# Kernel tuning notes

Hardware: AMD Instinct MI355X
Metric: run time of the kernel (lower is better)

The kernel has to match this reference:

```python
import jax, jax.numpy as jnp
import numpy as np
import math

D_MODEL = 512
N_HEADS = 8
K_NEIGHBORS = 30
B, S = 4, 2048
N_VARIATES = 8
EPS = 1e-5


def layer_norm(x, g, b):
    m = jnp.mean(x, axis=-1, keepdims=True)
    v = jnp.mean(jnp.square(x - m), axis=-1, keepdims=True)
    return (x - m) * jax.lax.rsqrt(v + EPS) * g + b


def mha(x, mask, w_in, b_in, w_out, b_out):
    # x: [B,S,D]; mask: [B,S,S] bool, True = blocked (same for every head)
    Bb, Ss, D = x.shape
    H, dh = N_HEADS, D // N_HEADS
    qkv = x @ w_in.T + b_in                      # [B,S,3D]
    q, k, v = jnp.split(qkv, 3, axis=-1)
    q = q.reshape(Bb, Ss, H, dh).transpose(0, 2, 1, 3)
    k = k.reshape(Bb, Ss, H, dh).transpose(0, 2, 1, 3)
    v = v.reshape(Bb, Ss, H, dh).transpose(0, 2, 1, 3)
    scores = jnp.einsum('bhqd,bhkd->bhqk', q, k) / math.sqrt(dh)
    scores = jnp.where(mask[:, None, :, :], -jnp.inf, scores)
    attn = jax.nn.softmax(scores, axis=-1)
    o = jnp.einsum('bhqk,bhkd->bhqd', attn, v)
    o = o.transpose(0, 2, 1, 3).reshape(Bb, Ss, D)
    return o @ w_out.T + b_out


def build_masks(variates, times, valid_mask):
    Bb, Ss = variates.shape
    eye = jnp.eye(Ss, dtype=bool)
    same_var = variates[:, :, None] == variates[:, None, :]      # [B,S,S]
    valid_2d = valid_mask[:, :, None] & valid_mask[:, None, :]
    intra_mask = ~(same_var & valid_2d)                          # True = blocked
    blocked_i = jnp.any(jnp.all(intra_mask, axis=-1))
    intra_mask = intra_mask & ~(blocked_i & eye)                 # unblock diagonal if any row fully blocked

    diff_var = ~same_var
    time_dist = jnp.abs(times[:, :, None] - times[:, None, :])
    time_dist = jnp.where(~valid_2d | ~diff_var, jnp.inf, time_dist)
    k = min(K_NEIGHBORS, Ss)
    _, topk_idx = jax.lax.top_k(-time_dist, k)                   # k smallest distances
    b_idx = jnp.arange(Bb)[:, None, None]
    r_idx = jnp.arange(Ss)[None, :, None]
    knn_mask = jnp.zeros((Bb, Ss, Ss), dtype=bool).at[b_idx, r_idx, topk_idx].set(True)
    knn_mask = knn_mask & valid_2d
    inter_mask = ~knn_mask
    blocked_e = jnp.any(jnp.all(inter_mask, axis=-1))
    inter_mask = inter_mask & ~(blocked_e & eye)
    return intra_mask, inter_mask


def setup_inputs() -> dict:
    key = jax.random.key(0)
    ks = jax.random.split(key, 12)
    D = D_MODEL
    s = 0.02
    inp = {
        'x': jax.random.normal(ks[0], (B, S, D), dtype=jnp.float32),
        'variates': jax.random.randint(ks[1], (B, S), 0, N_VARIATES),
        'times': jax.random.uniform(ks[2], (B, S), dtype=jnp.float32),
        'valid_mask': jnp.ones((B, S), dtype=bool),
        'in_w1': jax.random.normal(ks[3], (3 * D, D), dtype=jnp.float32) * s,
        'in_b1': jnp.zeros((3 * D,), dtype=jnp.float32),
        'out_w1': jax.random.normal(ks[4], (D, D), dtype=jnp.float32) * s,
        'out_b1': jnp.zeros((D,), dtype=jnp.float32),
        'ln_g1': jnp.ones((D,), dtype=jnp.float32),
        'ln_b1': jnp.zeros((D,), dtype=jnp.float32),
        'in_w2': jax.random.normal(ks[5], (3 * D, D), dtype=jnp.float32) * s,
        'in_b2': jnp.zeros((3 * D,), dtype=jnp.float32),
        'out_w2': jax.random.normal(ks[6], (D, D), dtype=jnp.float32) * s,
        'out_b2': jnp.zeros((D,), dtype=jnp.float32),
        'ln_g2': jnp.ones((D,), dtype=jnp.float32),
        'ln_b2': jnp.zeros((D,), dtype=jnp.float32),
    }
    return inp


def reference(x, variates, times, valid_mask,
              in_w1, in_b1, out_w1, out_b1, ln_g1, ln_b1,
              in_w2, in_b2, out_w2, out_b2, ln_g2, ln_b2):
    intra_mask, inter_mask = build_masks(variates, times, valid_mask)
    a1 = mha(x, intra_mask, in_w1, in_b1, out_w1, out_b1)
    x = layer_norm(x + a1, ln_g1, ln_b1)
    a2 = mha(x, inter_mask, in_w2, in_b2, out_w2, out_b2)
    x = layer_norm(x + a2, ln_g2, ln_b2)
    return x
```

## Files before the change

### kernel.cpp

```cpp
#include <hip/hip_runtime.h>


#define S_LEN 2048
#define BATCH 4
#define DM    512
#define NH    8
#define DH    64
#define KNN_K 30
#define NVAR  8
#define NTOK  (BATCH * S_LEN)
#define QKVD  (3 * DM)
#define PADCAP 2560
#define MAXTILE 40

typedef float f32x4 __attribute__((ext_vector_type(4)));
typedef short s16x8 __attribute__((ext_vector_type(8)));
typedef short s16x4 __attribute__((ext_vector_type(4)));

__device__ __forceinline__ float bf2f(short u) {
  return __uint_as_float(((unsigned)(unsigned short)u) << 16);
}
__device__ __forceinline__ short f2bf(float f) {
  unsigned x = __float_as_uint(f);
  return (short)((x + 0x7fffu + ((x >> 16) & 1u)) >> 16);
}

#define KNNB (NTOK / 8)
#define C_N0 (NTOK * DM / 4)
#define C_N1 (QKVD * DM / 4)
#define C_N2 (DM * DM / 4)
#define C_B1 (C_N0 + C_N1)
#define C_B2 (C_B1 + C_N2)
#define C_B3 (C_B2 + C_N1)
#define C_B4 (C_B3 + C_N2)
#define PREP_GRID (KNNB + BATCH + C_B4 / 256)

__global__ __launch_bounds__(256) void prep_all(
    const int* __restrict__ variates, const float* __restrict__ times,
    int* __restrict__ knn_out,
    int* __restrict__ gcnt, int* __restrict__ pgoff, int* __restrict__ porig,
    int* __restrict__ tileV, int* __restrict__ tileQ0, int* __restrict__ ntile,
    const float* __restrict__ s0, const float* __restrict__ s1,
    const float* __restrict__ s2, const float* __restrict__ s3,
    const float* __restrict__ s4, short* __restrict__ d0,
    short* __restrict__ d1, short* __restrict__ d2,
    short* __restrict__ d3, short* __restrict__ d4) {
  int blk = blockIdx.x;
  int tid = threadIdx.x;

  if (blk < KNNB) {
    int w = tid >> 6, lane = tid & 63;
    int bq0 = blk * 8 + w * 2;
    int bq1 = bq0 + 1;
    int b = bq0 >> 11;
    float tq0 = times[bq0], tq1 = times[bq1];
    int vq0 = variates[bq0], vq1 = variates[bq1];
    const float* tb = times + b * S_LEN;
    const int* vb = variates + b * S_LEN;
    int j0 = lane * 32;

    unsigned u0[32], u1[32];
#pragma unroll
    for (int q = 0; q < 8; ++q) {
      float4 t4 = *(const float4*)(tb + j0 + q * 4);
      int4 v4 = *(const int4*)(vb + j0 + q * 4);
      u0[q * 4 + 0] = __float_as_uint((v4.x == vq0) ? __builtin_inff() : fabsf(tq0 - t4.x));
      u0[q * 4 + 1] = __float_as_uint((v4.y == vq0) ? __builtin_inff() : fabsf(tq0 - t4.y));
      u0[q * 4 + 2] = __float_as_uint((v4.z == vq0) ? __builtin_inff() : fabsf(tq0 - t4.z));
      u0[q * 4 + 3] = __float_as_uint((v4.w == vq0) ? __builtin_inff() : fabsf(tq0 - t4.w));
      u1[q * 4 + 0] = __float_as_uint((v4.x == vq1) ? __builtin_inff() : fabsf(tq1 - t4.x));
      u1[q * 4 + 1] = __float_as_uint((v4.y == vq1) ? __builtin_inff() : fabsf(tq1 - t4.y));
      u1[q * 4 + 2] = __float_as_uint((v4.z == vq1) ? __builtin_inff() : fabsf(tq1 - t4.z));
      u1[q * 4 + 3] = __float_as_uint((v4.w == vq1) ? __builtin_inff() : fabsf(tq1 - t4.w));
    }

    unsigned lo0 = 0u, hi0 = 0x7F800000u;
    unsigned lo1 = 0u, hi1 = 0x7F800000u;
    for (int it = 0; it < 31; ++it) {
      unsigned mid0 = lo0 + ((hi0 - lo0) >> 1);
      unsigned mid1 = lo1 + ((hi1 - lo1) >> 1);
      int c0 = 0, c1 = 0;
#pragma unroll
      for (int k = 0; k < 32; ++k) {
        c0 += (u0[k] <= mid0) ? 1 : 0;
        c1 += (u1[k] <= mid1) ? 1 : 0;
      }
      int pc = c0 | (c1 << 16);
#pragma unroll
      for (int o2 = 32; o2; o2 >>= 1) pc += __shfl_xor(pc, o2);
      int pc0 = pc & 0xffff, pc1 = pc >> 16;
      if (lo0 < hi0) { if (pc0 >= KNN_K) hi0 = mid0; else lo0 = mid0 + 1; }
      if (lo1 < hi1) { if (pc1 >= KNN_K) hi1 = mid1; else lo1 = mid1 + 1; }
    }
    unsigned tau0 = lo0, tau1 = lo1;

    int cl0 = 0, ce0 = 0, cl1 = 0, ce1 = 0;
#pragma unroll
    for (int k = 0; k < 32; ++k) {
      cl0 += (u0[k] < tau0) ? 1 : 0;  ce0 += (u0[k] == tau0) ? 1 : 0;
      cl1 += (u1[k] < tau1) ? 1 : 0;  ce1 += (u1[k] == tau1) ? 1 : 0;
    }
    int pa = cl0 | (cl1 << 16), pe = ce0 | (ce1 << 16);
#pragma unroll
    for (int o2 = 1; o2 < 64; o2 <<= 1) {
      int ta = __shfl_up(pa, o2);
      int te = __shfl_up(pe, o2);
      if (lane >= o2) { pa += ta; pe += te; }
    }
    int paTop = __shfl(pa, 63);
    int totL0 = paTop & 0xffff, totL1 = paTop >> 16;
    int excl0 = (pa & 0xffff) - cl0, excl1 = (pa >> 16) - cl1;
    int exce0 = totL0 + (pe & 0xffff) - ce0, exce1 = totL1 + (pe >> 16) - ce1;

    int* op0 = knn_out + bq0 * KNN_K;
    int* op1 = knn_out + bq1 * KNN_K;
    int pos0 = excl0, pos1 = excl1;
#pragma unroll
    for (int k = 0; k < 32; ++k) {
      if (u0[k] < tau0) { op0[pos0] = j0 + k; ++pos0; }
      if (u1[k] < tau1) { op1[pos1] = j0 + k; ++pos1; }
    }
    int r0 = exce0, r1 = exce1;
#pragma unroll
    for (int k = 0; k < 32; ++k) {
      if (u0[k] == tau0) { if (r0 < KNN_K) op0[r0] = j0 + k; ++r0; }
      if (u1[k] == tau1) { if (r1 < KNN_K) op1[r1] = j0 + k; ++r1; }
    }
  } else if (blk < KNNB + BATCH) {
    int b = blk - KNNB;
    int t = tid;
    __shared__ int scnt[64][NVAR];
    __shared__ int soff[64][NVAR];
    __shared__ int stot[NVAR], sbase[NVAR];
    for (int p = t; p < PADCAP; p += 256) porig[b * PADCAP + p] = -1;
    const int* vb = variates + b * S_LEN;
    int c[NVAR] = {0, 0, 0, 0, 0, 0, 0, 0};
    if (t < 64) {
      for (int j = t * 32; j < t * 32 + 32; ++j) {
        int v = vb[j];
#pragma unroll
        for (int u = 0; u < NVAR; ++u) c[u] += (v == u);
      }
#pragma unroll
      for (int u = 0; u < NVAR; ++u) scnt[t][u] = c[u];
    }
    __syncthreads();
    if (t < NVAR) {
      int a = 0;
      for (int u = 0; u < 64; ++u) { soff[u][t] = a; a += scnt[u][t]; }
      stot[t] = a;
    }
    __syncthreads();
    if (t == 0) {
      int a = 0, nt = 0;
      for (int v = 0; v < NVAR; ++v) {
        sbase[v] = a;
        pgoff[b * NVAR + v] = a;
        gcnt[b * NVAR + v] = stot[v];
        int ntv = (stot[v] + 63) >> 6;
        for (int i = 0; i < ntv; ++i) {
          tileV[b * MAXTILE + nt] = v;
          tileQ0[b * MAXTILE + nt] = a + i * 64;
          ++nt;
        }
        a += ntv * 64;
      }
      ntile[b] = nt;
    }
    __syncthreads();
    if (t < 64) {
      int o[NVAR];
#pragma unroll
      for (int u = 0; u < NVAR; ++u) o[u] = sbase[u] + soff[t][u];
      for (int j = t * 32; j < t * 32 + 32; ++j) {
        int v = vb[j];
        int dst = 0;
#pragma unroll
        for (int u = 0; u < NVAR; ++u) dst += (v == u) ? o[u] : 0;
        porig[b * PADCAP + dst] = j;
#pragma unroll
        for (int u = 0; u < NVAR; ++u) o[u] += (v == u);
      }
    }
  } else {
    int i = (blk - KNNB - BATCH) * 256 + tid;
    const float* src; short* dst; int k;
    if (i < C_N0)      { src = s0; dst = d0; k = i; }
    else if (i < C_B1) { src = s1; dst = d1; k = i - C_N0; }
    else if (i < C_B2) { src = s2; dst = d2; k = i - C_B1; }
    else if (i < C_B3) { src = s3; dst = d3; k = i - C_B2; }
    else               { src = s4; dst = d4; k = i - C_B3; }
    float4 v = ((const float4*)src)[k];
    s16x4 o;
    o[0] = f2bf(v.x); o[1] = f2bf(v.y); o[2] = f2bf(v.z); o[3] = f2bf(v.w);
    ((s16x4*)dst)[k] = o;
  }
}

template <int OUT_BF16>
__global__ __launch_bounds__(256) void gemm_bt(const short* __restrict__ A,
                                               const short* __restrict__ Bm,
                                               const float* __restrict__ bias,
                                               void* __restrict__ Cout,
                                               int M, int N, int K) {
  __shared__ short sA[128 * 40];
  __shared__ short sB[128 * 40];
  int n0 = blockIdx.x * 128, m0 = blockIdx.y * 128;
  int tid = threadIdx.x;
  int lane = tid & 63, wv = tid >> 6;
  int wr = wv >> 1, wc = wv & 1;

  int srow = tid >> 2;
  int scol = (tid & 3) * 8;
  const short* aG = A + (size_t)(m0 + srow) * K + scol;
  const short* bG = Bm + (size_t)(n0 + srow) * K + scol;

  f32x4 acc[4][4] = {};
  int nk = K >> 5;

  s16x8 pa0 = *(const s16x8*)(aG);
  s16x8 pa1 = *(const s16x8*)(aG + (size_t)64 * K);
  s16x8 pb0 = *(const s16x8*)(bG);
  s16x8 pb1 = *(const s16x8*)(bG + (size_t)64 * K);

  for (int kt = 0; kt < nk; ++kt) {
    __syncthreads();
    *(s16x8*)&sA[srow * 40 + scol] = pa0;
    *(s16x8*)&sA[(srow + 64) * 40 + scol] = pa1;
    *(s16x8*)&sB[srow * 40 + scol] = pb0;
    *(s16x8*)&sB[(srow + 64) * 40 + scol] = pb1;
    __syncthreads();
    if (kt + 1 < nk) {
      const short* a2 = aG + (kt + 1) * 32;
      const short* b2 = bG + (kt + 1) * 32;
      pa0 = *(const s16x8*)(a2);
      pa1 = *(const s16x8*)(a2 + (size_t)64 * K);
      pb0 = *(const s16x8*)(b2);
      pb1 = *(const s16x8*)(b2 + (size_t)64 * K);
    }
    int kb = (lane >> 4) * 8;
    int ar = wr * 64 + (lane & 15);
    int br = wc * 64 + (lane & 15);
    s16x8 af[4], bf[4];
#pragma unroll
    for (int m = 0; m < 4; ++m) af[m] = *(const s16x8*)&sA[(ar + m * 16) * 40 + kb];
#pragma unroll
    for (int n = 0; n < 4; ++n) bf[n] = *(const s16x8*)&sB[(br + n * 16) * 40 + kb];
#pragma unroll
    for (int m = 0; m < 4; ++m)
#pragma unroll
      for (int n = 0; n < 4; ++n)
        acc[m][n] = __builtin_amdgcn_mfma_f32_16x16x32_bf16(af[m], bf[n], acc[m][n], 0, 0, 0);
  }

  int crow0 = m0 + wr * 64 + ((lane >> 4) * 4);
  int ccol0 = n0 + wc * 64 + (lane & 15);
#pragma unroll
  for (int n = 0; n < 4; ++n) {
    int col = ccol0 + n * 16;
    float bv = bias ? bias[col] : 0.f;
#pragma unroll
    for (int m = 0; m < 4; ++m) {
#pragma unroll
      for (int j = 0; j < 4; ++j) {
        int row = crow0 + m * 16 + j;
        float val = acc[m][n][j] + bv;
        if (OUT_BF16)
          ((short*)Cout)[(size_t)row * N + col] = f2bf(val);
        else
          ((float*)Cout)[(size_t)row * N + col] = val;
      }
    }
  }
}

__global__ __launch_bounds__(192) void permute_qkv(const short* __restrict__ qkvb,
                                                   const int* __restrict__ porig,
                                                   short* __restrict__ pq) {
  int row = blockIdx.x;
  int b = row / PADCAP;
  int orig = porig[row];
  int t = threadIdx.x;
  s16x8 val;
  if (orig >= 0) {
    val = *(const s16x8*)(qkvb + ((size_t)(b * S_LEN + orig)) * QKVD + t * 8);
    if (t < 64) {
#pragma unroll
      for (int i = 0; i < 8; ++i) val[i] = f2bf(bf2f(val[i]) * 0.125f);
    }
  } else {
#pragma unroll
    for (int i = 0; i < 8; ++i) val[i] = 0;
  }
  *(s16x8*)(pq + (size_t)row * QKVD + t * 8) = val;
}

__global__ __launch_bounds__(256) void intra_attn(
    const short* __restrict__ pq, const int* __restrict__ porig,
    const int* __restrict__ tileV, const int* __restrict__ tileQ0,
    const int* __restrict__ ntile, const int* __restrict__ pgoff,
    const int* __restrict__ gcnt, short* __restrict__ o) {
  int b = blockIdx.z, h = blockIdx.y, t = blockIdx.x;
  if (t >= ntile[b]) return;
  int v = tileV[b * MAXTILE + t];
  int q0 = tileQ0[b * MAXTILE + t];
  int k0 = pgoff[b * NVAR + v];
  int L = gcnt[b * NVAR + v];
  int nch = (L + 63) >> 6;

  __shared__ short sQ[2][64][40];
  __shared__ short sK[2][64][40];
  __shared__ short sVT[2][64][40];
  __shared__ short sP[2][64][40];

  int tid = threadIdx.x, lane = tid & 63, w = tid >> 6;
  int colbase = lane & 15;
  int kfrag = (lane >> 4) * 8;

  {
    int r = tid >> 2, cc = (tid & 3) * 16;
    const short* src = pq + ((size_t)(b * PADCAP + q0 + r)) * QKVD + h * DH + cc;
    s16x8 v0 = *(const s16x8*)src;
    s16x8 v1 = *(const s16x8*)(src + 8);
    int half = cc >> 5, kk = cc & 31;
    *(s16x8*)&sQ[half][r][kk] = v0;
    *(s16x8*)&sQ[half][r][kk + 8] = v1;
  }

  f32x4 accO[4] = {};
  float mrun[4], lrun[4];
#pragma unroll
  for (int j = 0; j < 4; ++j) { mrun[j] = -__builtin_inff(); lrun[j] = 0.f; }

  for (int c = 0; c < nch; ++c) {
    __syncthreads();
    {
      int r = tid >> 2, cc = (tid & 3) * 16;
      size_t rowg = (size_t)(b * PADCAP + k0 + c * 64 + r) * QKVD;
      const short* srcK = pq + rowg + DM + h * DH + cc;
      s16x8 k0v = *(const s16x8*)srcK;
      s16x8 k1v = *(const s16x8*)(srcK + 8);
      int half = cc >> 5, kk = cc & 31;
      *(s16x8*)&sK[half][r][kk] = k0v;
      *(s16x8*)&sK[half][r][kk + 8] = k1v;
      const short* srcV = pq + rowg + 2 * DM + h * DH + cc;
      s16x8 v0v = *(const s16x8*)srcV;
      s16x8 v1v = *(const s16x8*)(srcV + 8);
      int khalf = r >> 5, kkv = r & 31;
#pragma unroll
      for (int i = 0; i < 8; ++i) sVT[khalf][cc + i][kkv] = v0v[i];
#pragma unroll
      for (int i = 0; i < 8; ++i) sVT[khalf][cc + 8 + i][kkv] = v1v[i];
    }
    __syncthreads();

    s16x8 aQ0 = *(const s16x8*)&sQ[0][w * 16 + colbase][kfrag];
    s16x8 aQ1 = *(const s16x8*)&sQ[1][w * 16 + colbase][kfrag];
    f32x4 accS[4] = {};
#pragma unroll
    for (int n = 0; n < 4; ++n) {
      s16x8 b0 = *(const s16x8*)&sK[0][n * 16 + colbase][kfrag];
      s16x8 b1 = *(const s16x8*)&sK[1][n * 16 + colbase][kfrag];
      accS[n] = __builtin_amdgcn_mfma_f32_16x16x32_bf16(aQ0, b0, accS[n], 0, 0, 0);
      accS[n] = __builtin_amdgcn_mfma_f32_16x16x32_bf16(aQ1, b1, accS[n], 0, 0, 0);
    }

    float pv[4][4];
#pragma unroll
    for (int j = 0; j < 4; ++j) {
      float cm = -__builtin_inff();
#pragma unroll
      for (int n = 0; n < 4; ++n) {
        bool ok = (c * 64 + n * 16 + colbase) < L;
        float se = ok ? accS[n][j] : -__builtin_inff();
        cm = fmaxf(cm, se);
      }
      for (int o2 = 8; o2; o2 >>= 1) cm = fmaxf(cm, __shfl_xor(cm, o2));
      float mn = fmaxf(mrun[j], cm);
      float al = __expf(mrun[j] - mn);
      float rs = 0.f;
#pragma unroll
      for (int n = 0; n < 4; ++n) {
        bool ok = (c * 64 + n * 16 + colbase) < L;
        float p = ok ? __expf(accS[n][j] - mn) : 0.f;
        pv[n][j] = p;
        rs += p;
      }
      for (int o2 = 8; o2; o2 >>= 1) rs += __shfl_xor(rs, o2);
      lrun[j] = lrun[j] * al + rs;
      mrun[j] = mn;
#pragma unroll
      for (int n = 0; n < 4; ++n) accO[n][j] *= al;
    }

    int prow = w * 16 + ((lane >> 4) << 2);
#pragma unroll
    for (int n = 0; n < 4; ++n)
#pragma unroll
      for (int j = 0; j < 4; ++j)
        sP[n >> 1][prow + j][colbase + ((n & 1) << 4)] = f2bf(pv[n][j]);

    s16x8 aP0 = *(const s16x8*)&sP[0][w * 16 + colbase][kfrag];
    s16x8 aP1 = *(const s16x8*)&sP[1][w * 16 + colbase][kfrag];
#pragma unroll
    for (int n = 0; n < 4; ++n) {
      s16x8 b0 = *(const s16x8*)&sVT[0][n * 16 + colbase][kfrag];
      s16x8 b1 = *(const s16x8*)&sVT[1][n * 16 + colbase][kfrag];
      accO[n] = __builtin_amdgcn_mfma_f32_16x16x32_bf16(aP0, b0, accO[n], 0, 0, 0);
      accO[n] = __builtin_amdgcn_mfma_f32_16x16x32_bf16(aP1, b1, accO[n], 0, 0, 0);
    }
  }

#pragma unroll
  for (int j = 0; j < 4; ++j) {
    int prow = w * 16 + (lane >> 4) * 4 + j;
    int orig = porig[b * PADCAP + q0 + prow];
    if (orig >= 0) {
      float inv = 1.f / lrun[j];
      size_t base = ((size_t)(b * S_LEN + orig)) * DM + h * DH;
#pragma unroll
      for (int n = 0; n < 4; ++n)
        o[base + n * 16 + colbase] = f2bf(accO[n][j] * inv);
    }
  }
}

__global__ __launch_bounds__(256) void inter_attn(const short* __restrict__ qkv,
                                                  const int* __restrict__ knn,
                                                  short* __restrict__ o) {
  __shared__ float sS[4][NH][32];
  __shared__ float sP[4][NH][32];
  int tid = threadIdx.x, lane = tid & 63, w = tid >> 6;
  int bq = blockIdx.x * 4 + w;
  int b = bq >> 11;
  int h = lane >> 3;

  int myidx = (lane < KNN_K) ? knn[bq * KNN_K + lane] : 0;

  s16x8 q8 = *(const s16x8*)(qkv + (size_t)bq * QKVD + lane * 8);
  float qf[8];
#pragma unroll
  for (int i = 0; i < 8; ++i) qf[i] = bf2f(q8[i]) * 0.125f;

  for (int j = 0; j < KNN_K; ++j) {
    int idx = __shfl(myidx, j);
    s16x8 k8 = *(const s16x8*)(qkv + ((size_t)(b * S_LEN + idx)) * QKVD + DM + lane * 8);
    float acc = 0.f;
#pragma unroll
    for (int i = 0; i < 8; ++i) acc += qf[i] * bf2f(k8[i]);
    acc += __shfl_xor(acc, 1);
    acc += __shfl_xor(acc, 2);
    acc += __shfl_xor(acc, 4);
    if ((lane & 7) == 0) sS[w][h][j] = acc;
  }

  int jsub = lane & 7;
  float sv0 = sS[w][h][jsub];
  float sv1 = sS[w][h][jsub + 8];
  float sv2 = sS[w][h][jsub + 16];
  float sv3 = (jsub < 6) ? sS[w][h][jsub + 24] : -__builtin_inff();
  float m = fmaxf(fmaxf(sv0, sv1), fmaxf(sv2, sv3));
  m = fmaxf(m, __shfl_xor(m, 1));
  m = fmaxf(m, __shfl_xor(m, 2));
  m = fmaxf(m, __shfl_xor(m, 4));
  float p0 = __expf(sv0 - m), p1 = __expf(sv1 - m), p2 = __expf(sv2 - m);
  float p3 = (jsub < 6) ? __expf(sv3 - m) : 0.f;
  sP[w][h][jsub] = p0;
  sP[w][h][jsub + 8] = p1;
  sP[w][h][jsub + 16] = p2;
  sP[w][h][jsub + 24] = p3;
  float l = p0 + p1 + p2 + p3;
  l += __shfl_xor(l, 1);
  l += __shfl_xor(l, 2);
  l += __shfl_xor(l, 4);

  float o8[8] = {};
  for (int j = 0; j < KNN_K; ++j) {
    int idx = __shfl(myidx, j);
    s16x8 v8 = *(const s16x8*)(qkv + ((size_t)(b * S_LEN + idx)) * QKVD + 2 * DM + lane * 8);
    float p = sP[w][h][j];
#pragma unroll
    for (int i = 0; i < 8; ++i) o8[i] += p * bf2f(v8[i]);
  }
  float inv = 1.f / l;
  s16x8 ov;
#pragma unroll
  for (int i = 0; i < 8; ++i) ov[i] = f2bf(o8[i] * inv);
  *(s16x8*)(o + (size_t)bq * DM + lane * 8) = ov;
}

__global__ __launch_bounds__(256) void residual_ln(const float* __restrict__ x,
                                                   const float* __restrict__ a,
                                                   const float* __restrict__ g,
                                                   const float* __restrict__ bta,
                                                   float* __restrict__ yf,
                                                   short* __restrict__ yb) {
  int row = blockIdx.x * 4 + (threadIdx.x >> 6);
  int lane = threadIdx.x & 63;
  const float4* xp = (const float4*)(x + (size_t)row * DM);
  const float4* ap = (const float4*)(a + (size_t)row * DM);
  float4 v0 = xp[lane * 2], v1 = xp[lane * 2 + 1];
  float4 a0 = ap[lane * 2], a1 = ap[lane * 2 + 1];
  float r[8] = {v0.x + a0.x, v0.y + a0.y, v0.z + a0.z, v0.w + a0.w,
                v1.x + a1.x, v1.y + a1.y, v1.z + a1.z, v1.w + a1.w};
  float s = 0.f;
#pragma unroll
  for (int j = 0; j < 8; ++j) s += r[j];
  for (int o2 = 32; o2; o2 >>= 1) s += __shfl_xor(s, o2);
  float mean = s * (1.f / DM);
  float vs = 0.f;
#pragma unroll
  for (int j = 0; j < 8; ++j) { float d = r[j] - mean; vs += d * d; }
  for (int o2 = 32; o2; o2 >>= 1) vs += __shfl_xor(vs, o2);
  float inv = rsqrtf(vs * (1.f / DM) + 1e-5f);
  const float4* gp = (const float4*)g;
  const float4* bp = (const float4*)bta;
  float4 g0 = gp[lane * 2], g1 = gp[lane * 2 + 1];
  float4 b0 = bp[lane * 2], b1 = bp[lane * 2 + 1];
  float gg[8] = {g0.x, g0.y, g0.z, g0.w, g1.x, g1.y, g1.z, g1.w};
  float bb[8] = {b0.x, b0.y, b0.z, b0.w, b1.x, b1.y, b1.z, b1.w};
  float y[8];
#pragma unroll
  for (int j = 0; j < 8; ++j) y[j] = (r[j] - mean) * inv * gg[j] + bb[j];
  float4 o0 = {y[0], y[1], y[2], y[3]};
  float4 o1 = {y[4], y[5], y[6], y[7]};
  float4* yp = (float4*)(yf + (size_t)row * DM);
  yp[lane * 2] = o0;
  yp[lane * 2 + 1] = o1;
  if (yb) {
    s16x8 ob;
#pragma unroll
    for (int j = 0; j < 8; ++j) ob[j] = f2bf(y[j]);
    *(s16x8*)(yb + (size_t)row * DM + lane * 8) = ob;
  }
}

extern "C" void kernel_launch(void* const* d_in, const int* in_sizes, int n_in,
                              void* d_out, int out_size, void* d_ws, size_t ws_size,
                              hipStream_t stream) {
  const float* x      = (const float*)d_in[0];
  const int*   var    = (const int*)d_in[1];
  const float* times  = (const float*)d_in[2];
  const float* in_w1  = (const float*)d_in[4];
  const float* in_b1  = (const float*)d_in[5];
  const float* out_w1 = (const float*)d_in[6];
  const float* out_b1 = (const float*)d_in[7];
  const float* ln_g1  = (const float*)d_in[8];
  const float* ln_b1  = (const float*)d_in[9];
  const float* in_w2  = (const float*)d_in[10];
  const float* in_b2  = (const float*)d_in[11];
  const float* out_w2 = (const float*)d_in[12];
  const float* out_b2 = (const float*)d_in[13];
  const float* ln_g2  = (const float*)d_in[14];
  const float* ln_b2  = (const float*)d_in[15];
  float* out = (float*)d_out;

  char* ws = (char*)d_ws;
  size_t off = 0;
  auto alloc = [&](size_t bytes) -> char* {
    char* p = ws + off;
    off = (off + bytes + 255) & ~(size_t)255;
    return p;
  };
  short* xb    = (short*)alloc((size_t)NTOK * DM * 2);
  short* x1b   = (short*)alloc((size_t)NTOK * DM * 2);
  short* w1q   = (short*)alloc((size_t)QKVD * DM * 2);
  short* w1o   = (short*)alloc((size_t)DM * DM * 2);
  short* w2q   = (short*)alloc((size_t)QKVD * DM * 2);
  short* w2o   = (short*)alloc((size_t)DM * DM * 2);
  short* qkvb  = (short*)alloc((size_t)NTOK * QKVD * 2);
  short* ob    = (short*)alloc((size_t)NTOK * DM * 2);
  char*  region = alloc((size_t)NTOK * DM * 4 * 2);
  float* af    = (float*)region;
  float* x1f   = (float*)(region + (size_t)NTOK * DM * 4);
  short* pqkv  = (short*)region;
  int* gcnt    = (int*)alloc((size_t)BATCH * NVAR * 4);
  int* pgoff   = (int*)alloc((size_t)BATCH * NVAR * 4);
  int* porig   = (int*)alloc((size_t)BATCH * PADCAP * 4);
  int* tileV   = (int*)alloc((size_t)BATCH * MAXTILE * 4);
  int* tileQ0  = (int*)alloc((size_t)BATCH * MAXTILE * 4);
  int* ntile   = (int*)alloc((size_t)BATCH * 4);
  int* knn     = (int*)alloc((size_t)NTOK * KNN_K * 4);

  prep_all<<<PREP_GRID, 256, 0, stream>>>(
      var, times, knn, gcnt, pgoff, porig, tileV, tileQ0, ntile,
      x, in_w1, out_w1, in_w2, out_w2, xb, w1q, w1o, w2q, w2o);

  gemm_bt<1><<<dim3(QKVD / 128, NTOK / 128), 256, 0, stream>>>(xb, w1q, in_b1, qkvb,
                                                               NTOK, QKVD, DM);
  permute_qkv<<<BATCH * PADCAP, 192, 0, stream>>>(qkvb, porig, pqkv);
  intra_attn<<<dim3(MAXTILE, NH, BATCH), 256, 0, stream>>>(pqkv, porig, tileV, tileQ0,
                                                           ntile, pgoff, gcnt, ob);
  gemm_bt<0><<<dim3(DM / 128, NTOK / 128), 256, 0, stream>>>(ob, w1o, out_b1, af,
                                                             NTOK, DM, DM);
  residual_ln<<<NTOK / 4, 256, 0, stream>>>(x, af, ln_g1, ln_b1, x1f, x1b);

  gemm_bt<1><<<dim3(QKVD / 128, NTOK / 128), 256, 0, stream>>>(x1b, w2q, in_b2, qkvb,
                                                               NTOK, QKVD, DM);
  inter_attn<<<NTOK / 4, 256, 0, stream>>>(qkvb, knn, ob);
  gemm_bt<0><<<dim3(DM / 128, NTOK / 128), 256, 0, stream>>>(ob, w2o, out_b2, af,
                                                             NTOK, DM, DM);
  residual_ln<<<NTOK / 4, 256, 0, stream>>>(x1f, af, ln_g2, ln_b2, out, nullptr);
}
```

Baseline: 226.3 us.

## Gather QKV rows in intra-attention directly and stop kNN bisection early

Removes the permute_qkv kernel, which copied QKV rows into variate-grouped padded order with Q pre-scaled. intra_attn now looks up each row's original token through porig and loads Q/K/V straight from the GEMM output, and applies the 1/sqrt(dh) scale to the scores in fp32. This saves a full launch plus a write and read of the permuted buffer, at the cost of scattered gathers inside attention. Padded rows are clamped to token 0, which the existing length mask is relied on to exclude. The kNN threshold bisection also now exits once both searches have converged.

After: 220.8 us. 1.02x faster.

```diff
diff --git a/kernel.cpp b/kernel.cpp
--- a/kernel.cpp
+++ b/kernel.cpp
@@ -91,6 +91,7 @@
       int pc0 = pc & 0xffff, pc1 = pc >> 16;
       if (lo0 < hi0) { if (pc0 >= KNN_K) hi0 = mid0; else lo0 = mid0 + 1; }
       if (lo1 < hi1) { if (pc1 >= KNN_K) hi1 = mid1; else lo1 = mid1 + 1; }
+      if (lo0 >= hi0 && lo1 >= hi1) break;
     }
     unsigned tau0 = lo0, tau1 = lo1;
 
@@ -274,29 +275,8 @@
   }
 }
 
-__global__ __launch_bounds__(192) void permute_qkv(const short* __restrict__ qkvb,
-                                                   const int* __restrict__ porig,
-                                                   short* __restrict__ pq) {
-  int row = blockIdx.x;
-  int b = row / PADCAP;
-  int orig = porig[row];
-  int t = threadIdx.x;
-  s16x8 val;
-  if (orig >= 0) {
-    val = *(const s16x8*)(qkvb + ((size_t)(b * S_LEN + orig)) * QKVD + t * 8);
-    if (t < 64) {
-#pragma unroll
-      for (int i = 0; i < 8; ++i) val[i] = f2bf(bf2f(val[i]) * 0.125f);
-    }
-  } else {
-#pragma unroll
-    for (int i = 0; i < 8; ++i) val[i] = 0;
-  }
-  *(s16x8*)(pq + (size_t)row * QKVD + t * 8) = val;
-}
-
 __global__ __launch_bounds__(256) void intra_attn(
-    const short* __restrict__ pq, const int* __restrict__ porig,
+    const short* __restrict__ qkv, const int* __restrict__ porig,
     const int* __restrict__ tileV, const int* __restrict__ tileQ0,
     const int* __restrict__ ntile, const int* __restrict__ pgoff,
     const int* __restrict__ gcnt, short* __restrict__ o) {
@@ -319,7 +299,9 @@
 
   {
     int r = tid >> 2, cc = (tid & 3) * 16;
-    const short* src = pq + ((size_t)(b * PADCAP + q0 + r)) * QKVD + h * DH + cc;
+    int tok = porig[b * PADCAP + q0 + r];
+    if (tok < 0) tok = 0;
+    const short* src = qkv + ((size_t)(b * S_LEN + tok)) * QKVD + h * DH + cc;
     s16x8 v0 = *(const s16x8*)src;
     s16x8 v1 = *(const s16x8*)(src + 8);
     int half = cc >> 5, kk = cc & 31;
@@ -336,14 +318,16 @@
     __syncthreads();
     {
       int r = tid >> 2, cc = (tid & 3) * 16;
-      size_t rowg = (size_t)(b * PADCAP + k0 + c * 64 + r) * QKVD;
-      const short* srcK = pq + rowg + DM + h * DH + cc;
+      int tok = porig[b * PADCAP + k0 + c * 64 + r];
+      if (tok < 0) tok = 0;
+      size_t rowg = (size_t)(b * S_LEN + tok) * QKVD;
+      const short* srcK = qkv + rowg + DM + h * DH + cc;
       s16x8 k0v = *(const s16x8*)srcK;
       s16x8 k1v = *(const s16x8*)(srcK + 8);
       int half = cc >> 5, kk = cc & 31;
       *(s16x8*)&sK[half][r][kk] = k0v;
       *(s16x8*)&sK[half][r][kk + 8] = k1v;
-      const short* srcV = pq + rowg + 2 * DM + h * DH + cc;
+      const short* srcV = qkv + rowg + 2 * DM + h * DH + cc;
       s16x8 v0v = *(const s16x8*)srcV;
       s16x8 v1v = *(const s16x8*)(srcV + 8);
       int khalf = r >> 5, kkv = r & 31;
@@ -364,6 +348,10 @@
       accS[n] = __builtin_amdgcn_mfma_f32_16x16x32_bf16(aQ0, b0, accS[n], 0, 0, 0);
       accS[n] = __builtin_amdgcn_mfma_f32_16x16x32_bf16(aQ1, b1, accS[n], 0, 0, 0);
     }
+#pragma unroll
+    for (int n = 0; n < 4; ++n)
+#pragma unroll
+      for (int j = 0; j < 4; ++j) accS[n][j] *= 0.125f;
 
     float pv[4][4];
 #pragma unroll
@@ -570,10 +558,8 @@
   short* w2o   = (short*)alloc((size_t)DM * DM * 2);
   short* qkvb  = (short*)alloc((size_t)NTOK * QKVD * 2);
   short* ob    = (short*)alloc((size_t)NTOK * DM * 2);
-  char*  region = alloc((size_t)NTOK * DM * 4 * 2);
-  float* af    = (float*)region;
-  float* x1f   = (float*)(region + (size_t)NTOK * DM * 4);
-  short* pqkv  = (short*)region;
+  float* af    = (float*)alloc((size_t)NTOK * DM * 4);
+  float* x1f   = (float*)alloc((size_t)NTOK * DM * 4);
   int* gcnt    = (int*)alloc((size_t)BATCH * NVAR * 4);
   int* pgoff   = (int*)alloc((size_t)BATCH * NVAR * 4);
   int* porig   = (int*)alloc((size_t)BATCH * PADCAP * 4);
@@ -588,8 +574,7 @@
 
   gemm_bt<1><<<dim3(QKVD / 128, NTOK / 128), 256, 0, stream>>>(xb, w1q, in_b1, qkvb,
                                                                NTOK, QKVD, DM);
-  permute_qkv<<<BATCH * PADCAP, 192, 0, stream>>>(qkvb, porig, pqkv);
-  intra_attn<<<dim3(MAXTILE, NH, BATCH), 256, 0, stream>>>(pqkv, porig, tileV, tileQ0,
+  intra_attn<<<dim3(MAXTILE, NH, BATCH), 256, 0, stream>>>(qkvb, porig, tileV, tileQ0,
                                                            ntile, pgoff, gcnt, ob);
   gemm_bt<0><<<dim3(DM / 128, NTOK / 128), 256, 0, stream>>>(ob, w1o, out_b1, af,
                                                              NTOK, DM, DM);
```
